# Kernel tuning notes

Measured on AMD Instinct MI355X. Metric: run time of the kernel, lower is better.

## Reference

```python
import jax, jax.numpy as jnp
import numpy as np

C_Z = 128
C_HIDDEN = 32
N_HEAD = 4
HC = N_HEAD * C_HIDDEN  # 128
LN_EPS = 1e-5


def setup_inputs() -> dict:
    key = jax.random.key(0)
    ks = jax.random.split(key, 8)
    b, n = 1, 256
    s = 1.0 / np.sqrt(C_Z)
    return {
        "z_ij": jax.random.normal(ks[0], (b, n, n, C_Z), dtype=jnp.float32),
        "ln_gamma": jnp.ones((C_Z,), dtype=jnp.float32),
        "ln_beta": jnp.zeros((C_Z,), dtype=jnp.float32),
        "Wq": jax.random.normal(ks[1], (C_Z, HC), dtype=jnp.float32) * s,
        "Wk": jax.random.normal(ks[2], (C_Z, HC), dtype=jnp.float32) * s,
        "Wv": jax.random.normal(ks[3], (C_Z, HC), dtype=jnp.float32) * s,
        "Wb": jax.random.normal(ks[4], (C_Z, N_HEAD), dtype=jnp.float32) * s,
        "Wg": jax.random.normal(ks[5], (C_Z, HC), dtype=jnp.float32) * s,
        "Wout": jax.random.normal(ks[6], (HC, C_Z), dtype=jnp.float32) * (1.0 / np.sqrt(HC)),
    }


def reference(z_ij, ln_gamma, ln_beta, Wq, Wk, Wv, Wb, Wg, Wout):
    b, n, _, _ = z_ij.shape
    # LayerNorm over c_z
    mu = jnp.mean(z_ij, axis=-1, keepdims=True)
    var = jnp.var(z_ij, axis=-1, keepdims=True)
    z = (z_ij - mu) * jax.lax.rsqrt(var + LN_EPS) * ln_gamma + ln_beta

    def heads(x):  # [b,i,j,hc] -> [b,i,j,h,d]
        return x.reshape(b, n, n, N_HEAD, C_HIDDEN)

    q = heads(z @ Wq)
    k = heads(z @ Wk)
    v = heads(z @ Wv)
    bias = z @ Wb                      # [b,i,j,h]
    g = jax.nn.sigmoid(heads(z @ Wg))  # [b,i,j,h,d]

    scores = jnp.einsum('bijhd,bikhd->bijkh', q, k) / np.sqrt(C_HIDDEN)
    scores = scores + bias[:, None]    # bias[b, j, k, h] broadcast over i
    a = jax.nn.softmax(scores, axis=-2)  # over k
    o = jnp.einsum('bijkh,bikhd->bijhd', a, v)
    o = (g * o).reshape(b, n, n, HC)
    return o @ Wout
```

## Files before the change

### kernel.cpp

```cpp
#include <hip/hip_runtime.h>

typedef _Float16 f16x8 __attribute__((ext_vector_type(8)));
typedef _Float16 f16x2 __attribute__((ext_vector_type(2)));
typedef float f32x4 __attribute__((ext_vector_type(4)));

#define MFMA16(a, b, c) __builtin_amdgcn_mfma_f32_16x16x32_f16(a, b, c, 0, 0, 0)

#define NROW 65536
#define SEGB 16777216ull
#define LOG2E 1.4426950408889634f

__global__ __launch_bounds__(256) void k_ln(
    const float* __restrict__ z, const float* __restrict__ gamma,
    const float* __restrict__ beta, const float* __restrict__ Wb,
    const float* __restrict__ Wq, const float* __restrict__ Wk,
    const float* __restrict__ Wv, const float* __restrict__ Wg,
    const float* __restrict__ Wout,
    _Float16* __restrict__ zln, float* __restrict__ biasT,
    _Float16* __restrict__ WtAll)
{
  __shared__ _Float16 sw[32 * 136];
  int bid = blockIdx.x;
  if (bid < 16384) {
    int lane = threadIdx.x & 63;
    int w = threadIdx.x >> 6;
    int row = bid * 4 + w;
    float2 v = ((const float2*)(z + (size_t)row * 128))[lane];
    float s = v.x + v.y;
    #pragma unroll
    for (int m = 1; m < 64; m <<= 1) s += __shfl_xor(s, m);
    float mu = s * 0.0078125f;
    float dx = v.x - mu, dy = v.y - mu;
    float q = dx * dx + dy * dy;
    #pragma unroll
    for (int m = 1; m < 64; m <<= 1) q += __shfl_xor(q, m);
    float rs = rsqrtf(q * 0.0078125f + 1e-5f);
    float2 g2 = ((const float2*)gamma)[lane];
    float2 b2 = ((const float2*)beta)[lane];
    float y0 = dx * rs * g2.x + b2.x;
    float y1 = dy * rs * g2.y + b2.y;
    f16x2 pr; pr.x = (_Float16)y0; pr.y = (_Float16)y1;
    *(f16x2*)(zln + (size_t)row * 128 + 2 * lane) = pr;
  } else if (bid < 16384 + 20) {
    int t = bid - 16384;
    int mat = t >> 2, n0 = (t & 3) * 32;
    const float* src = (mat == 0) ? Wq : (mat == 1) ? Wk : (mat == 2) ? Wv
                       : (mat == 3) ? Wg : Wout;
    _Float16* dst = WtAll + ((mat == 4) ? 5 : mat) * 16384;
    for (int it = 0; it < 16; ++it) {
      int e = threadIdx.x + it * 256;
      int c = e >> 5, j = e & 31;
      sw[j * 136 + c] = (_Float16)src[c * 128 + n0 + j];
    }
    __syncthreads();
    for (int it = 0; it < 2; ++it) {
      int ch = threadIdx.x + it * 256;
      int n = ch >> 4, k8 = (ch & 15) * 8;
      *(int4*)(dst + (n0 + n) * 128 + k8) = *(const int4*)&sw[n * 136 + k8];
    }
  } else {
    _Float16* dst = WtAll + 4 * 16384;
    for (int e = threadIdx.x; e < 16384; e += 256) {
      int n = e >> 7, k = e & 127;
      dst[e] = (n < 4) ? (_Float16)Wb[k * 4 + n] : (_Float16)0.f;
    }
  }
}

__global__ __launch_bounds__(256) void k_proj(
    const _Float16* __restrict__ A, const _Float16* __restrict__ WtAll,
    _Float16* __restrict__ Qb, _Float16* __restrict__ Kb,
    _Float16* __restrict__ Vb, _Float16* __restrict__ Gb,
    float* __restrict__ biasT)
{
  __shared__ _Float16 sA[128 * 136];
  __shared__ _Float16 sB[128 * 136];
  int e = blockIdx.x;
  int xcd = e & 7;
  int t = e >> 3;
  int by = t % 5;
  int g = t / 5;
  int m0 = (g * 8 + xcd) * 128;
  const _Float16* Bt = WtAll + by * 16384;
  _Float16* outp = (by == 0) ? Qb : (by == 1) ? Kb : (by == 2) ? Vb : Gb;
  int tid = threadIdx.x;
  for (int it = 0; it < 8; ++it) {
    int ch = tid + it * 256;
    int r = ch >> 4, c8 = (ch & 15) * 8;
    *(int4*)&sA[r * 136 + c8] = *(const int4*)(A + (size_t)(m0 + r) * 128 + c8);
    *(int4*)&sB[r * 136 + c8] = *(const int4*)(Bt + r * 128 + c8);
  }
  __syncthreads();
  int lane = tid & 63, w = tid >> 6;
  int mw = (w >> 1) * 64, nw = (w & 1) * 64;
  int lr = lane & 15, lg = lane >> 4;
  int ntm = (by == 4) ? 1 : 4;
  f32x4 z4 = {0.f, 0.f, 0.f, 0.f};
  f32x4 acc[4][4];
  #pragma unroll
  for (int mt = 0; mt < 4; ++mt)
    #pragma unroll
    for (int nt = 0; nt < 4; ++nt) acc[mt][nt] = z4;
  #pragma unroll
  for (int k0 = 0; k0 < 128; k0 += 32) {
    f16x8 af[4], bf[4];
    #pragma unroll
    for (int mt = 0; mt < 4; ++mt)
      af[mt] = *(const f16x8*)&sA[(mw + mt * 16 + lr) * 136 + k0 + lg * 8];
    #pragma unroll
    for (int nt = 0; nt < 4; ++nt)
      if (nt < ntm)
        bf[nt] = *(const f16x8*)&sB[(nw + nt * 16 + lr) * 136 + k0 + lg * 8];
    #pragma unroll
    for (int mt = 0; mt < 4; ++mt)
      #pragma unroll
      for (int nt = 0; nt < 4; ++nt)
        if (nt < ntm)
          acc[mt][nt] = MFMA16(af[mt], bf[nt], acc[mt][nt]);
  }
  if (by == 4) {
    if (nw == 0 && lr < 4) {
      #pragma unroll
      for (int mt = 0; mt < 4; ++mt)
        #pragma unroll
        for (int r = 0; r < 4; ++r) {
          int row = m0 + mw + mt * 16 + lg * 4 + r;
          biasT[(size_t)lr * NROW + row] = acc[mt][0][r] * LOG2E;
        }
    }
    return;
  }
  bool sig = (by == 3);
  #pragma unroll
  for (int mt = 0; mt < 4; ++mt)
    #pragma unroll
    for (int nt = 0; nt < 4; ++nt)
      #pragma unroll
      for (int r = 0; r < 4; ++r) {
        int row = m0 + mw + mt * 16 + lg * 4 + r;
        int col = nw + nt * 16 + lr;
        float v = acc[mt][nt][r];
        if (sig) v = 1.0f / (1.0f + __expf(-v));
        outp[(size_t)row * 128 + col] = (_Float16)v;
      }
}

__global__ __launch_bounds__(256) void k_attn(
    const _Float16* __restrict__ Qb, const _Float16* __restrict__ Kb,
    const _Float16* __restrict__ Vb, const _Float16* __restrict__ Gb,
    const float* __restrict__ biasT, _Float16* __restrict__ OG)
{
  __shared__ _Float16 sK[256 * 32];
  __shared__ _Float16 sV[32 * 256];
  __shared__ _Float16 sP[64 * 256];
  int i = blockIdx.x, h = blockIdx.y;
  int tid = threadIdx.x;
  size_t base = ((size_t)i * 256) * 128 + h * 32;
  for (int it = 0; it < 4; ++it) {
    int ch = tid + it * 256;
    int r = ch >> 2, cx = ch & 3;
    int p = cx ^ ((r >> 1) & 3);
    *(int4*)&sK[r * 32 + p * 8] = *(const int4*)(Kb + base + (size_t)r * 128 + cx * 8);
  }
  for (int it = 0; it < 4; ++it) {
    int ch = tid + it * 256;
    int k = ch >> 2, d8 = (ch & 3) * 8;
    f16x8 tv = *(const f16x8*)(Vb + base + (size_t)k * 128 + d8);
    #pragma unroll
    for (int jj = 0; jj < 8; ++jj) {
      int d = d8 + jj;
      int p = (k >> 3) ^ (d & 7);
      sV[d * 256 + p * 8 + (k & 7)] = tv[jj];
    }
  }
  __syncthreads();
  int lane = tid & 63, w = tid >> 6;
  int lr = lane & 15, lg = lane >> 4;
  const float scale = 0.2550348858f;
  f32x4 z4 = {0.f, 0.f, 0.f, 0.f};
  for (int pass = 0; pass < 4; ++pass) {
    int jbase = pass * 64;
    int jq = jbase + w * 16 + lr;
    f16x8 aq = *(const f16x8*)(Qb + base + (size_t)jq * 128 + lg * 8);
    f32x4 sacc[16];
    __builtin_amdgcn_s_setprio(1);
    #pragma unroll
    for (int kt = 0; kt < 16; ++kt) {
      int r = kt * 16 + lr;
      int p = lg ^ ((r >> 1) & 3);
      f16x8 bk = *(const f16x8*)&sK[r * 32 + p * 8];
      sacc[kt] = MFMA16(aq, bk, z4);
    }
    __builtin_amdgcn_s_setprio(0);
    #pragma unroll
    for (int r = 0; r < 4; ++r) {
      int j = jbase + w * 16 + lg * 4 + r;
      const float* brow = biasT + (size_t)h * NROW + (size_t)j * 256;
      float mx = -1e30f;
      #pragma unroll
      for (int kt = 0; kt < 16; ++kt) {
        float sv = sacc[kt][r] * scale + brow[kt * 16 + lr];
        sacc[kt][r] = sv;
        mx = fmaxf(mx, sv);
      }
      #pragma unroll
      for (int msk = 1; msk < 16; msk <<= 1) mx = fmaxf(mx, __shfl_xor(mx, msk));
      float sum = 0.f;
      #pragma unroll
      for (int kt = 0; kt < 16; ++kt) {
        float pv = exp2f(sacc[kt][r] - mx);
        sacc[kt][r] = pv;
        sum += pv;
      }
      #pragma unroll
      for (int msk = 1; msk < 16; msk <<= 1) sum += __shfl_xor(sum, msk);
      float rinv = 1.0f / sum;
      int row = w * 16 + lg * 4 + r;
      #pragma unroll
      for (int kt = 0; kt < 16; ++kt) {
        int k = kt * 16 + lr;
        int pch = (k >> 3) ^ (row & 7);
        sP[row * 256 + pch * 8 + (k & 7)] = (_Float16)(sacc[kt][r] * rinv);
      }
    }
    f32x4 oacc[2] = {z4, z4};
    int prow = w * 16 + lr;
    #pragma unroll
    for (int ks = 0; ks < 8; ++ks) {
      int c = ks * 4 + lg;
      f16x8 ap = *(const f16x8*)&sP[prow * 256 + (c ^ (prow & 7)) * 8];
      __builtin_amdgcn_s_setprio(1);
      #pragma unroll
      for (int nt = 0; nt < 2; ++nt) {
        int d = nt * 16 + lr;
        f16x8 bv = *(const f16x8*)&sV[d * 256 + (c ^ (d & 7)) * 8];
        oacc[nt] = MFMA16(ap, bv, oacc[nt]);
      }
      __builtin_amdgcn_s_setprio(0);
    }
    #pragma unroll
    for (int nt = 0; nt < 2; ++nt)
      #pragma unroll
      for (int r = 0; r < 4; ++r) {
        int j = jbase + w * 16 + lg * 4 + r;
        int d = nt * 16 + lr;
        size_t idx = base + (size_t)j * 128 + d;
        float g = (float)Gb[idx];
        OG[idx] = (_Float16)(oacc[nt][r] * g);
      }
  }
}

__global__ __launch_bounds__(256) void k_outp(
    const _Float16* __restrict__ A, const _Float16* __restrict__ Bt,
    float* __restrict__ out)
{
  __shared__ _Float16 sA[128 * 136];
  __shared__ _Float16 sB[128 * 136];
  int m0 = blockIdx.x * 128;
  int tid = threadIdx.x;
  for (int it = 0; it < 8; ++it) {
    int ch = tid + it * 256;
    int r = ch >> 4, c8 = (ch & 15) * 8;
    *(int4*)&sA[r * 136 + c8] = *(const int4*)(A + (size_t)(m0 + r) * 128 + c8);
    *(int4*)&sB[r * 136 + c8] = *(const int4*)(Bt + r * 128 + c8);
  }
  __syncthreads();
  int lane = tid & 63, w = tid >> 6;
  int mw = (w >> 1) * 64, nw = (w & 1) * 64;
  int lr = lane & 15, lg = lane >> 4;
  f32x4 z4 = {0.f, 0.f, 0.f, 0.f};
  f32x4 acc[4][4];
  #pragma unroll
  for (int mt = 0; mt < 4; ++mt)
    #pragma unroll
    for (int nt = 0; nt < 4; ++nt) acc[mt][nt] = z4;
  #pragma unroll
  for (int k0 = 0; k0 < 128; k0 += 32) {
    f16x8 af[4], bf[4];
    #pragma unroll
    for (int mt = 0; mt < 4; ++mt)
      af[mt] = *(const f16x8*)&sA[(mw + mt * 16 + lr) * 136 + k0 + lg * 8];
    #pragma unroll
    for (int nt = 0; nt < 4; ++nt)
      bf[nt] = *(const f16x8*)&sB[(nw + nt * 16 + lr) * 136 + k0 + lg * 8];
    #pragma unroll
    for (int mt = 0; mt < 4; ++mt)
      #pragma unroll
      for (int nt = 0; nt < 4; ++nt)
        acc[mt][nt] = MFMA16(af[mt], bf[nt], acc[mt][nt]);
  }
  #pragma unroll
  for (int mt = 0; mt < 4; ++mt)
    #pragma unroll
    for (int nt = 0; nt < 4; ++nt)
      #pragma unroll
      for (int r = 0; r < 4; ++r) {
        int row = m0 + mw + mt * 16 + lg * 4 + r;
        int col = nw + nt * 16 + lr;
        out[(size_t)row * 128 + col] = acc[mt][nt][r];
      }
}

extern "C" void kernel_launch(void* const* d_in, const int* in_sizes, int n_in,
                              void* d_out, int out_size, void* d_ws, size_t ws_size,
                              hipStream_t stream) {
  (void)in_sizes; (void)n_in; (void)out_size; (void)ws_size;
  const float* z    = (const float*)d_in[0];
  const float* gam  = (const float*)d_in[1];
  const float* bet  = (const float*)d_in[2];
  const float* Wq   = (const float*)d_in[3];
  const float* Wk   = (const float*)d_in[4];
  const float* Wv   = (const float*)d_in[5];
  const float* Wb   = (const float*)d_in[6];
  const float* Wg   = (const float*)d_in[7];
  const float* Wout = (const float*)d_in[8];

  char* ws = (char*)d_ws;
  _Float16* zln   = (_Float16*)(ws);
  _Float16* Qb    = (_Float16*)(ws + SEGB);
  _Float16* Kb    = (_Float16*)(ws + SEGB * 2);
  _Float16* Vb    = (_Float16*)(ws + SEGB * 3);
  _Float16* Gb    = (_Float16*)(ws + SEGB * 4);
  float*    biasT = (float*)   (ws + SEGB * 5);
  _Float16* WtAll = (_Float16*)(ws + SEGB * 5 + 1048576);

  k_ln<<<16405, 256, 0, stream>>>(z, gam, bet, Wb, Wq, Wk, Wv, Wg, Wout,
                                  zln, biasT, WtAll);
  k_proj<<<2560, 256, 0, stream>>>(zln, WtAll, Qb, Kb, Vb, Gb, biasT);
  k_attn<<<dim3(256, 4), 256, 0, stream>>>(Qb, Kb, Vb, Gb, biasT, zln);
  k_outp<<<512, 256, 0, stream>>>(zln, WtAll + 5 * 16384, (float*)d_out);
}
```

Measured before the change: 193.4 us.

## Permute key ordering to vectorize bias loads and P stores, defer softmax normalization

Bias is stored with a permuted key index (k_lo*16+k_hi), so each lane reads its 16 bias values as four float4 loads instead of 16 strided scalar loads. The V tile in shared memory is permuted the same way, so the P row from each lane becomes two contiguous f16x8 stores rather than 16 scalar half stores. The 1/sum scaling moves from P to the output epilogue. This cuts global and LDS instruction counts in the softmax section, at the cost of unnormalized fp16 probabilities, which stay within 1 because the row max is subtracted, and a coupled layout across two kernels.

```diff
diff --git a/kernel.cpp b/kernel.cpp
--- a/kernel.cpp
+++ b/kernel.cpp
@@ -125,7 +125,9 @@
         #pragma unroll
         for (int r = 0; r < 4; ++r) {
           int row = m0 + mw + mt * 16 + lg * 4 + r;
-          biasT[(size_t)lr * NROW + row] = acc[mt][0][r] * LOG2E;
+          int lowk = row & 255;
+          int pos = (row & ~255) | ((lowk & 15) << 4) | (lowk >> 4);
+          biasT[(size_t)lr * NROW + pos] = acc[mt][0][r] * LOG2E;
         }
     }
     return;
@@ -166,11 +168,13 @@
     int ch = tid + it * 256;
     int k = ch >> 2, d8 = (ch & 3) * 8;
     f16x8 tv = *(const f16x8*)(Vb + base + (size_t)k * 128 + d8);
+    int k2 = ((k & 15) << 4) | (k >> 4);
+    int c2 = k2 >> 3, e2 = k2 & 7;
     #pragma unroll
     for (int jj = 0; jj < 8; ++jj) {
       int d = d8 + jj;
-      int p = (k >> 3) ^ (d & 7);
-      sV[d * 256 + p * 8 + (k & 7)] = tv[jj];
+      int p = c2 ^ (d & 7);
+      sV[d * 256 + p * 8 + e2] = tv[jj];
     }
   }
   __syncthreads();
@@ -192,36 +196,39 @@
       sacc[kt] = MFMA16(aq, bk, z4);
     }
     __builtin_amdgcn_s_setprio(0);
+    float rinv4[4];
     #pragma unroll
     for (int r = 0; r < 4; ++r) {
       int j = jbase + w * 16 + lg * 4 + r;
-      const float* brow = biasT + (size_t)h * NROW + (size_t)j * 256;
+      const float* brow = biasT + (size_t)h * NROW + (size_t)j * 256 + lr * 16;
+      float4 b4[4];
+      #pragma unroll
+      for (int m = 0; m < 4; ++m) b4[m] = ((const float4*)brow)[m];
       float mx = -1e30f;
       #pragma unroll
       for (int kt = 0; kt < 16; ++kt) {
-        float sv = sacc[kt][r] * scale + brow[kt * 16 + lr];
+        float bb = ((const float*)&b4[kt >> 2])[kt & 3];
+        float sv = sacc[kt][r] * scale + bb;
         sacc[kt][r] = sv;
         mx = fmaxf(mx, sv);
       }
       #pragma unroll
       for (int msk = 1; msk < 16; msk <<= 1) mx = fmaxf(mx, __shfl_xor(mx, msk));
       float sum = 0.f;
+      f16x8 h0, h1;
       #pragma unroll
       for (int kt = 0; kt < 16; ++kt) {
         float pv = exp2f(sacc[kt][r] - mx);
-        sacc[kt][r] = pv;
         sum += pv;
+        if (kt < 8) h0[kt] = (_Float16)pv;
+        else        h1[kt - 8] = (_Float16)pv;
       }
       #pragma unroll
       for (int msk = 1; msk < 16; msk <<= 1) sum += __shfl_xor(sum, msk);
-      float rinv = 1.0f / sum;
+      rinv4[r] = 1.0f / sum;
       int row = w * 16 + lg * 4 + r;
-      #pragma unroll
-      for (int kt = 0; kt < 16; ++kt) {
-        int k = kt * 16 + lr;
-        int pch = (k >> 3) ^ (row & 7);
-        sP[row * 256 + pch * 8 + (k & 7)] = (_Float16)(sacc[kt][r] * rinv);
-      }
+      *(f16x8*)&sP[row * 256 + ((2 * lr) ^ (row & 7)) * 8] = h0;
+      *(f16x8*)&sP[row * 256 + ((2 * lr + 1) ^ (row & 7)) * 8] = h1;
     }
     f32x4 oacc[2] = {z4, z4};
     int prow = w * 16 + lr;
@@ -246,7 +253,7 @@
         int d = nt * 16 + lr;
         size_t idx = base + (size_t)j * 128 + d;
         float g = (float)Gb[idx];
-        OG[idx] = (_Float16)(oacc[nt][r] * g);
+        OG[idx] = (_Float16)(oacc[nt][r] * rinv4[r] * g);
       }
   }
 }
```

Result: no change. 192.0 us (-0.7%).
